# Kernel optimization log

Measured on AMD Instinct MI355X. Metric: run time of the kernel, lower is better.

The kernel has to match this reference:

```python
import jax, jax.numpy as jnp
import numpy as np

N, L, H1, H2 = 20000, 64, 128, 128  # nodes, max_len==input_dim, hidden_dim1, hidden_dim2


def setup_inputs() -> dict:
    key = jax.random.key(0)
    ks = jax.random.split(key, 12)
    sample_matrix = jax.random.normal(ks[0], (N, L, L), dtype=jnp.float32)
    sample_mask = jax.random.randint(ks[1], (N, L, L), 0, 2).astype(jnp.int32)
    sample_mask = sample_mask.at[:, :, 0].set(1)  # keep at least one valid logit per row
    # gather_idx[n, 0] = 0 (self prob); gather_idx[n, j] = position of node in neighbor j's list + 1
    gather_idx = jax.random.randint(ks[2], (N, L), 0, L).astype(jnp.int32)
    gather_idx = gather_idx.at[:, 0].set(0)
    # row_valid[n, j] = 1 iff j <= degree(n); rows past the degree stay 0 in middle_matrix
    row_valid = jax.random.randint(ks[3], (N, L), 0, 2).astype(jnp.int32)
    row_valid = row_valid.at[:, 0].set(1)
    s1 = np.float32(1.0 / np.sqrt(L))
    s2 = np.float32(1.0 / np.sqrt(H1))
    W1 = jax.random.normal(ks[4], (L, H1), dtype=jnp.float32) * s1
    b1 = jnp.zeros((H1,), jnp.float32)
    W2 = jax.random.normal(ks[5], (H1, L), dtype=jnp.float32) * s2
    b2 = jnp.zeros((L,), jnp.float32)
    W3 = jax.random.normal(ks[6], (L, H2), dtype=jnp.float32) * s1
    b3 = jnp.zeros((H2,), jnp.float32)
    W4 = jax.random.normal(ks[7], (H2, 1), dtype=jnp.float32) * s2
    b4 = jnp.zeros((1,), jnp.float32)
    return {
        "sample_matrix": sample_matrix, "sample_mask": sample_mask,
        "gather_idx": gather_idx, "row_valid": row_valid,
        "W1": W1, "b1": b1, "W2": W2, "b2": b2,
        "W3": W3, "b3": b3, "W4": W4, "b4": b4,
    }


def reference(sample_matrix, sample_mask, gather_idx, row_valid,
              W1, b1, W2, b2, W3, b3, W4, b4):
    # Per-(node,row) MLP: fc1 -> relu -> fc2, masked softmax over max_len (dropout is eval-mode identity)
    h = jax.nn.relu(jnp.einsum('nrk,kh->nrh', sample_matrix, W1) + b1)   # [N, L, H1]
    logits = jnp.einsum('nrh,hk->nrk', h, W2) + b2                        # [N, L, L]
    logits = jnp.where(sample_mask == 0, -jnp.inf, logits)
    probs = jax.nn.softmax(logits, axis=-1)                               # [N, L, L]
    # middle_matrix: row 0 takes prob[0], row j takes prob at the neighbor's back-pointer position
    mid = jnp.take_along_axis(probs, gather_idx[:, :, None], axis=2)[:, :, 0]  # [N, L]
    mid = jnp.where(row_valid == 1, mid, jnp.float32(0.0))                # unfilled rows stay 0
    mid = jnp.where(jnp.isnan(mid), jnp.float32(0.0), mid)                # all-masked softmax -> NaN -> 0
    y = jax.nn.relu(mid @ W3 + b3)                                        # [N, H2]
    out = jax.nn.sigmoid(y @ W4 + b4)                                     # [N, 1]
    return out.reshape(-1)
```

## Files before the change

kernel.cpp:

```cpp
#include <hip/hip_runtime.h>
#include <hip/hip_bf16.h>

typedef __attribute__((ext_vector_type(8))) __bf16 bf16x8;
typedef __attribute__((ext_vector_type(4))) float f32x4;

#define NN 20000
#define GRID1 1024
#define NSLOT 1024

__global__ void pack_w(const float* __restrict__ W1, const float* __restrict__ W2,
                       __bf16* __restrict__ w1p, __bf16* __restrict__ w2p) {
    int i = blockIdx.x * 256 + threadIdx.x;
    if (i < 64 * 128) {
        int c = i >> 6, k = i & 63;
        w1p[i] = (__bf16)W1[k * 128 + c];
        int c2 = i >> 7, k2 = i & 127;
        w2p[i] = (__bf16)W2[k2 * 64 + c2];
    }
}

struct NodeBuf { float4 sx[4]; int4 mv[4]; int gi; int rv; };

__global__ __launch_bounds__(256, 4) void vpsl_stage1p(
    const float* __restrict__ S, const int* __restrict__ mask,
    const int* __restrict__ gidx, const int* __restrict__ rvalid,
    const __bf16* __restrict__ w1p, const __bf16* __restrict__ w2p,
    const float* __restrict__ b1, const float* __restrict__ b2,
    float* __restrict__ midg)
{
    __shared__ __align__(16) __bf16 w1_lds[128 * 64];
    __shared__ __align__(16) __bf16 w2_lds[64 * 128];
    __shared__ __align__(16) __bf16 h_lds[4][16][136];

    const int tid  = threadIdx.x;
    const int w    = tid >> 6;
    const int lane = tid & 63;
    const int g    = lane >> 4;
    const int lc   = lane & 15;
    const int swz  = (lc & 7) << 4;

    for (int c = tid; c < 1024; c += 256) {
        int b = c * 16;
        int r1 = b >> 7, o1 = b & 127;
        *reinterpret_cast<float4*>(reinterpret_cast<char*>(w1_lds) + r1 * 128 + (o1 ^ ((r1 & 7) << 4)))
            = reinterpret_cast<const float4*>(w1p)[c];
        int r2 = b >> 8, o2 = b & 255;
        *reinterpret_cast<float4*>(reinterpret_cast<char*>(w2_lds) + r2 * 256 + (o2 ^ ((r2 & 7) << 4)))
            = reinterpret_cast<const float4*>(w2p)[c];
    }

    float b1v[8];
#pragma unroll
    for (int t = 0; t < 8; ++t) b1v[t] = b1[t * 16 + lc];
    float4 b2v4[4];
#pragma unroll
    for (int tm = 0; tm < 4; ++tm) b2v4[tm] = *reinterpret_cast<const float4*>(b2 + 16 * tm + 4 * g);

    __syncthreads();

    const int r = 16 * w + lc;
    const char* wc1 = reinterpret_cast<const char*>(w1_lds);
    const char* wc2 = reinterpret_cast<const char*>(w2_lds);

    auto LOADRV = [&](int2& rg, int node) {
        rg.x = rvalid[node * 64 + r];
        rg.y = gidx[node * 64 + r];
    };

    auto LOADNODE = [&](NodeBuf& nb, int node, int2 rg) {
        nb.rv = rg.x;
        nb.gi = rg.y;
        if (rg.x != 0) {
            const float* srow = S + ((size_t)node * 64 + r) * 64 + g * 8;
            nb.sx[0] = *reinterpret_cast<const float4*>(srow);
            nb.sx[1] = *reinterpret_cast<const float4*>(srow + 4);
            nb.sx[2] = *reinterpret_cast<const float4*>(srow + 32);
            nb.sx[3] = *reinterpret_cast<const float4*>(srow + 36);
            const int* mrow = mask + ((size_t)node * 64 + r) * 64 + 4 * g;
#pragma unroll
            for (int tm = 0; tm < 4; ++tm)
                nb.mv[tm] = *reinterpret_cast<const int4*>(mrow + 16 * tm);
        } else {
            float4 z4 = (float4){0.f, 0.f, 0.f, 0.f};
            int4   zi = (int4){0, 0, 0, 0};
#pragma unroll
            for (int q = 0; q < 4; ++q) { nb.sx[q] = z4; nb.mv[q] = zi; }
        }
    };

    auto COMPUTE = [&](const NodeBuf& nb, int node) {
        bf16x8 af[2];
#pragma unroll
        for (int ks = 0; ks < 2; ++ks) {
            bf16x8 a;
            a[0] = (__bf16)nb.sx[2 * ks].x; a[1] = (__bf16)nb.sx[2 * ks].y;
            a[2] = (__bf16)nb.sx[2 * ks].z; a[3] = (__bf16)nb.sx[2 * ks].w;
            a[4] = (__bf16)nb.sx[2 * ks + 1].x; a[5] = (__bf16)nb.sx[2 * ks + 1].y;
            a[6] = (__bf16)nb.sx[2 * ks + 1].z; a[7] = (__bf16)nb.sx[2 * ks + 1].w;
            af[ks] = a;
        }

#pragma unroll
        for (int t = 0; t < 8; ++t) {
            f32x4 acc = (f32x4){0.f, 0.f, 0.f, 0.f};
#pragma unroll
            for (int ks = 0; ks < 2; ++ks) {
                bf16x8 bw = *reinterpret_cast<const bf16x8*>(
                    wc1 + (t * 16 + lc) * 128 + ((ks * 64 + g * 16) ^ swz));
                acc = __builtin_amdgcn_mfma_f32_16x16x32_bf16(af[ks], bw, acc, 0, 0, 0);
            }
#pragma unroll
            for (int j = 0; j < 4; ++j) {
                float v = acc[j] + b1v[t];
                v = v > 0.f ? v : 0.f;
                h_lds[w][4 * g + j][16 * t + lc] = (__bf16)v;
            }
        }

        f32x4 lacc[4];
#pragma unroll
        for (int tm = 0; tm < 4; ++tm) lacc[tm] = (f32x4){0.f, 0.f, 0.f, 0.f};
#pragma unroll
        for (int ks = 0; ks < 4; ++ks) {
            bf16x8 ah = *reinterpret_cast<const bf16x8*>(&h_lds[w][lc][ks * 32 + g * 8]);
#pragma unroll
            for (int tm = 0; tm < 4; ++tm) {
                bf16x8 bw = *reinterpret_cast<const bf16x8*>(
                    wc2 + (tm * 16 + lc) * 256 + ((ks * 64 + g * 16) ^ swz));
                lacc[tm] = __builtin_amdgcn_mfma_f32_16x16x32_bf16(bw, ah, lacc[tm], 0, 0, 0);
            }
        }

        float l[4][4];
        float mt[4];
#pragma unroll
        for (int tm = 0; tm < 4; ++tm) {
            const int4  m4 = nb.mv[tm];
            const float4 bb = b2v4[tm];
            l[tm][0] = m4.x ? (lacc[tm][0] + bb.x) : -3.0e38f;
            l[tm][1] = m4.y ? (lacc[tm][1] + bb.y) : -3.0e38f;
            l[tm][2] = m4.z ? (lacc[tm][2] + bb.z) : -3.0e38f;
            l[tm][3] = m4.w ? (lacc[tm][3] + bb.w) : -3.0e38f;
            mt[tm] = fmaxf(fmaxf(l[tm][0], l[tm][1]), fmaxf(l[tm][2], l[tm][3]));
        }
        float mx = fmaxf(fmaxf(mt[0], mt[1]), fmaxf(mt[2], mt[3]));
        mx = fmaxf(mx, __shfl_xor(mx, 16));
        mx = fmaxf(mx, __shfl_xor(mx, 32));

        float st[4];
#pragma unroll
        for (int tm = 0; tm < 4; ++tm) {
#pragma unroll
            for (int j = 0; j < 4; ++j) l[tm][j] = __expf(l[tm][j] - mx);
            st[tm] = (l[tm][0] + l[tm][1]) + (l[tm][2] + l[tm][3]);
        }
        float s = (st[0] + st[1]) + (st[2] + st[3]);
        s += __shfl_xor(s, 16);
        s += __shfl_xor(s, 32);

        const int gi = nb.gi;
        float sel = 0.f;
#pragma unroll
        for (int tm = 0; tm < 4; ++tm)
#pragma unroll
            for (int j = 0; j < 4; ++j)
                sel += (gi == (16 * tm + 4 * g + j)) ? l[tm][j] : 0.f;
        sel += __shfl_xor(sel, 16);
        sel += __shfl_xor(sel, 32);

        if (g == 0) {
            float mval = (nb.rv != 0 && s > 0.f) ? (sel / s) : 0.f;
            midg[(size_t)node * 64 + r] = mval;
        }
    };

    int node = blockIdx.x;
    NodeBuf A, B;
    int2 rgA, rgB, rgT;
    rgT.x = 0; rgT.y = 0;
    LOADRV(rgA, node);
    if (node + NSLOT < NN) LOADRV(rgB, node + NSLOT); else { rgB.x = 0; rgB.y = 0; }
    LOADNODE(A, node, rgA);
    for (;;) {
        int n1 = node + NSLOT;
        int n2 = node + 2 * NSLOT;
        if (n2 < NN) LOADRV(rgT, n2);
        if (n1 < NN) LOADNODE(B, n1, rgB);
        COMPUTE(A, node);
        if (n1 >= NN) break;
        node = n1;
        n1 = node + NSLOT;
        n2 = node + 2 * NSLOT;
        if (n2 < NN) LOADRV(rgB, n2);
        if (n1 < NN) LOADNODE(A, n1, rgT);
        COMPUTE(B, node);
        if (n1 >= NN) break;
        node = n1;
    }
}

__global__ __launch_bounds__(256) void vpsl_stage2(
    const float* __restrict__ midg, const float* __restrict__ W3,
    const float* __restrict__ b3, const float* __restrict__ W4,
    const float* __restrict__ b4, float* __restrict__ out)
{
    __shared__ float mid_lds[2][64];
    __shared__ float red[2][128];
    const int tid = threadIdx.x;
    const int b = blockIdx.x;
    if (tid < 128) mid_lds[tid >> 6][tid & 63] = midg[(size_t)b * 128 + tid];
    __syncthreads();
    const int half = tid >> 7;
    const int t = tid & 127;
    float acc = 0.f;
#pragma unroll 8
    for (int k = 0; k < 64; ++k) acc += mid_lds[half][k] * W3[k * 128 + t];
    acc += b3[t];
    acc = acc > 0.f ? acc : 0.f;
    red[half][t] = acc * W4[t];
    __syncthreads();
    if ((tid & 127) < 64) {
        const int h2 = tid >> 7;
        const int tt = tid & 63;
        float v = red[h2][tt] + red[h2][tt + 64];
#pragma unroll
        for (int off = 1; off < 64; off <<= 1) v += __shfl_xor(v, off);
        if (tt == 0) out[b * 2 + h2] = 1.f / (1.f + __expf(-(v + b4[0])));
    }
}

__global__ __launch_bounds__(256) void vpsl_fused(
    const float* __restrict__ S, const int* __restrict__ mask,
    const int* __restrict__ gidx, const int* __restrict__ rvalid,
    const __bf16* __restrict__ w1p, const __bf16* __restrict__ w2p,
    const float* __restrict__ b1, const float* __restrict__ b2,
    const float* __restrict__ W3, const float* __restrict__ b3,
    const float* __restrict__ W4, const float* __restrict__ b4,
    float* __restrict__ out)
{
    __shared__ __align__(16) __bf16 h_lds[4][16][136];
    __shared__ float mid_s[64];
    __shared__ int   gi_s[64];
    __shared__ int   rv_s[64];
    __shared__ float red_s[128];

    const int n    = blockIdx.x;
    const int tid  = threadIdx.x;
    const int w    = tid >> 6;
    const int lane = tid & 63;
    const int g    = lane >> 4;
    const int lc   = lane & 15;

    if (tid < 64) {
        gi_s[tid] = gidx[(size_t)n * 64 + tid];
        rv_s[tid] = rvalid[(size_t)n * 64 + tid];
    }
    float b1v[8];
#pragma unroll
    for (int t = 0; t < 8; ++t) b1v[t] = b1[t * 16 + lc];
    float b2v[4];
#pragma unroll
    for (int t = 0; t < 4; ++t) b2v[t] = b2[t * 16 + lc];

    const float* srow = S + ((size_t)n * 64 + 16 * w + lc) * 64;
    bf16x8 af[2];
#pragma unroll
    for (int ks = 0; ks < 2; ++ks) {
        const float4* p = reinterpret_cast<const float4*>(srow + ks * 32 + g * 8);
        float4 x0 = p[0], x1 = p[1];
        bf16x8 a;
        a[0] = (__bf16)x0.x; a[1] = (__bf16)x0.y; a[2] = (__bf16)x0.z; a[3] = (__bf16)x0.w;
        a[4] = (__bf16)x1.x; a[5] = (__bf16)x1.y; a[6] = (__bf16)x1.z; a[7] = (__bf16)x1.w;
        af[ks] = a;
    }
    f32x4 hacc[8];
#pragma unroll
    for (int t = 0; t < 8; ++t) hacc[t] = (f32x4){0.f, 0.f, 0.f, 0.f};
#pragma unroll
    for (int ks = 0; ks < 2; ++ks)
#pragma unroll
        for (int t = 0; t < 8; ++t) {
            bf16x8 bf = *reinterpret_cast<const bf16x8*>(w1p + (t * 16 + lc) * 64 + ks * 32 + g * 8);
            hacc[t] = __builtin_amdgcn_mfma_f32_16x16x32_bf16(af[ks], bf, hacc[t], 0, 0, 0);
        }
#pragma unroll
    for (int t = 0; t < 8; ++t)
#pragma unroll
        for (int j = 0; j < 4; ++j) {
            float v = hacc[t][j] + b1v[t];
            v = v > 0.f ? v : 0.f;
            h_lds[w][4 * g + j][16 * t + lc] = (__bf16)v;
        }
    __syncthreads();

    f32x4 lacc[4];
#pragma unroll
    for (int t = 0; t < 4; ++t) lacc[t] = (f32x4){0.f, 0.f, 0.f, 0.f};
#pragma unroll
    for (int ks = 0; ks < 4; ++ks) {
        bf16x8 ah = *reinterpret_cast<const bf16x8*>(&h_lds[w][lc][ks * 32 + g * 8]);
#pragma unroll
        for (int t = 0; t < 4; ++t) {
            bf16x8 bf = *reinterpret_cast<const bf16x8*>(w2p + (t * 16 + lc) * 128 + ks * 32 + g * 8);
            lacc[t] = __builtin_amdgcn_mfma_f32_16x16x32_bf16(ah, bf, lacc[t], 0, 0, 0);
        }
    }
#pragma unroll
    for (int j = 0; j < 4; ++j) {
        const int row = 16 * w + 4 * g + j;
        const int* mrow = mask + ((size_t)n * 64 + row) * 64 + lc;
        int m[4];
#pragma unroll
        for (int t = 0; t < 4; ++t) m[t] = mrow[16 * t];
        float l[4];
#pragma unroll
        for (int t = 0; t < 4; ++t) l[t] = m[t] ? (lacc[t][j] + b2v[t]) : -3.0e38f;
        float mx = fmaxf(fmaxf(l[0], l[1]), fmaxf(l[2], l[3]));
#pragma unroll
        for (int off = 1; off < 16; off <<= 1) mx = fmaxf(mx, __shfl_xor(mx, off));
        float e[4];
#pragma unroll
        for (int t = 0; t < 4; ++t) e[t] = m[t] ? __expf(l[t] - mx) : 0.f;
        float s = (e[0] + e[1]) + (e[2] + e[3]);
#pragma unroll
        for (int off = 1; off < 16; off <<= 1) s += __shfl_xor(s, off);
        const int gi = gi_s[row];
        float sel = 0.f;
#pragma unroll
        for (int t = 0; t < 4; ++t) sel += (((gi >> 4) == t) && ((gi & 15) == lc)) ? e[t] : 0.f;
#pragma unroll
        for (int off = 1; off < 16; off <<= 1) sel += __shfl_xor(sel, off);
        if (lc == 0) {
            float mval = (rv_s[row] != 0 && s > 0.f) ? (sel / s) : 0.f;
            mid_s[row] = mval;
        }
    }
    __syncthreads();

    if (tid < 128) {
        float acc = 0.f;
#pragma unroll 8
        for (int k = 0; k < 64; ++k) acc += mid_s[k] * W3[k * 128 + tid];
        acc += b3[tid];
        acc = acc > 0.f ? acc : 0.f;
        red_s[tid] = acc * W4[tid];
    }
    __syncthreads();
    if (tid < 64) {
        float v = red_s[tid] + red_s[tid + 64];
#pragma unroll
        for (int off = 1; off < 64; off <<= 1) v += __shfl_xor(v, off);
        if (tid == 0) out[n] = 1.f / (1.f + __expf(-(v + b4[0])));
    }
}

extern "C" void kernel_launch(void* const* d_in, const int* in_sizes, int n_in,
                              void* d_out, int out_size, void* d_ws, size_t ws_size,
                              hipStream_t stream) {
    const float* S    = (const float*)d_in[0];
    const int*   mask = (const int*)d_in[1];
    const int*   gidx = (const int*)d_in[2];
    const int*   rv   = (const int*)d_in[3];
    const float* W1   = (const float*)d_in[4];
    const float* b1   = (const float*)d_in[5];
    const float* W2   = (const float*)d_in[6];
    const float* b2   = (const float*)d_in[7];
    const float* W3   = (const float*)d_in[8];
    const float* b3   = (const float*)d_in[9];
    const float* W4   = (const float*)d_in[10];
    const float* b4   = (const float*)d_in[11];
    float* out = (float*)d_out;

    __bf16* w1p = (__bf16*)d_ws;
    __bf16* w2p = w1p + 64 * 128;
    float*  midg = (float*)(w2p + 64 * 128);

    const size_t need = 2 * 64 * 128 * sizeof(__bf16) + (size_t)NN * 64 * sizeof(float);

    hipLaunchKernelGGL(pack_w, dim3(32), dim3(256), 0, stream, W1, W2, w1p, w2p);
    if (ws_size >= need) {
        hipLaunchKernelGGL(vpsl_stage1p, dim3(GRID1), dim3(256), 0, stream,
                           S, mask, gidx, rv, w1p, w2p, b1, b2, midg);
        hipLaunchKernelGGL(vpsl_stage2, dim3(NN / 2), dim3(256), 0, stream,
                           midg, W3, b3, W4, b4, out);
    } else {
        hipLaunchKernelGGL(vpsl_fused, dim3(NN), dim3(256), 0, stream,
                           S, mask, gidx, rv, w1p, w2p, b1, b2, W3, b3, W4, b4, out);
    }
}
```

Measured before the change: 143.9 us.

## Keep MLP weight fragments in registers instead of LDS, halve persistent grid

Loads the bf16 W1 and W2 MFMA operand fragments straight into per-thread registers (32 bf16x8 vectors) and drops the LDS weight copies, the swizzle and the block barrier. It also folds the b1/b2 bias adds into the MFMA accumulator initialisation. To fit the extra register pressure, launch bounds drop from 4 to 2 blocks per CU and the persistent grid is halved to 512 blocks. This removes LDS read traffic for the weights in the inner loop, at the cost of lower occupancy and less latency hiding for the streaming global loads.

After: 307.2 us. 114% more time.

```diff
diff --git a/kernel.cpp b/kernel.cpp
--- a/kernel.cpp
+++ b/kernel.cpp
@@ -5,8 +5,8 @@
 typedef __attribute__((ext_vector_type(4))) float f32x4;
 
 #define NN 20000
-#define GRID1 1024
-#define NSLOT 1024
+#define GRID1 512
+#define NSLOT 512
 
 __global__ void pack_w(const float* __restrict__ W1, const float* __restrict__ W2,
                        __bf16* __restrict__ w1p, __bf16* __restrict__ w2p) {
@@ -21,15 +21,13 @@
 
 struct NodeBuf { float4 sx[4]; int4 mv[4]; int gi; int rv; };
 
-__global__ __launch_bounds__(256, 4) void vpsl_stage1p(
+__global__ __launch_bounds__(256, 2) void vpsl_stage1p(
     const float* __restrict__ S, const int* __restrict__ mask,
     const int* __restrict__ gidx, const int* __restrict__ rvalid,
     const __bf16* __restrict__ w1p, const __bf16* __restrict__ w2p,
     const float* __restrict__ b1, const float* __restrict__ b2,
     float* __restrict__ midg)
 {
-    __shared__ __align__(16) __bf16 w1_lds[128 * 64];
-    __shared__ __align__(16) __bf16 w2_lds[64 * 128];
     __shared__ __align__(16) __bf16 h_lds[4][16][136];
 
     const int tid  = threadIdx.x;
@@ -37,17 +35,19 @@
     const int lane = tid & 63;
     const int g    = lane >> 4;
     const int lc   = lane & 15;
-    const int swz  = (lc & 7) << 4;
-
-    for (int c = tid; c < 1024; c += 256) {
-        int b = c * 16;
-        int r1 = b >> 7, o1 = b & 127;
-        *reinterpret_cast<float4*>(reinterpret_cast<char*>(w1_lds) + r1 * 128 + (o1 ^ ((r1 & 7) << 4)))
-            = reinterpret_cast<const float4*>(w1p)[c];
-        int r2 = b >> 8, o2 = b & 255;
-        *reinterpret_cast<float4*>(reinterpret_cast<char*>(w2_lds) + r2 * 256 + (o2 ^ ((r2 & 7) << 4)))
-            = reinterpret_cast<const float4*>(w2p)[c];
-    }
+
+    bf16x8 w1f[16];
+#pragma unroll
+    for (int t = 0; t < 8; ++t)
+#pragma unroll
+        for (int ks = 0; ks < 2; ++ks)
+            w1f[t * 2 + ks] = *reinterpret_cast<const bf16x8*>(w1p + (t * 16 + lc) * 64 + ks * 32 + g * 8);
+    bf16x8 w2f[16];
+#pragma unroll
+    for (int ks = 0; ks < 4; ++ks)
+#pragma unroll
+        for (int tm = 0; tm < 4; ++tm)
+            w2f[ks * 4 + tm] = *reinterpret_cast<const bf16x8*>(w2p + (tm * 16 + lc) * 128 + ks * 32 + g * 8);
 
     float b1v[8];
 #pragma unroll
@@ -56,11 +56,7 @@
 #pragma unroll
     for (int tm = 0; tm < 4; ++tm) b2v4[tm] = *reinterpret_cast<const float4*>(b2 + 16 * tm + 4 * g);
 
-    __syncthreads();
-
     const int r = 16 * w + lc;
-    const char* wc1 = reinterpret_cast<const char*>(w1_lds);
-    const char* wc2 = reinterpret_cast<const char*>(w2_lds);
 
     auto LOADRV = [&](int2& rg, int node) {
         rg.x = rvalid[node * 64 + r];
@@ -102,45 +98,37 @@
 
 #pragma unroll
         for (int t = 0; t < 8; ++t) {
-            f32x4 acc = (f32x4){0.f, 0.f, 0.f, 0.f};
-#pragma unroll
-            for (int ks = 0; ks < 2; ++ks) {
-                bf16x8 bw = *reinterpret_cast<const bf16x8*>(
-                    wc1 + (t * 16 + lc) * 128 + ((ks * 64 + g * 16) ^ swz));
-                acc = __builtin_amdgcn_mfma_f32_16x16x32_bf16(af[ks], bw, acc, 0, 0, 0);
-            }
+            f32x4 acc = (f32x4){b1v[t], b1v[t], b1v[t], b1v[t]};
+            acc = __builtin_amdgcn_mfma_f32_16x16x32_bf16(af[0], w1f[t * 2 + 0], acc, 0, 0, 0);
+            acc = __builtin_amdgcn_mfma_f32_16x16x32_bf16(af[1], w1f[t * 2 + 1], acc, 0, 0, 0);
 #pragma unroll
             for (int j = 0; j < 4; ++j) {
-                float v = acc[j] + b1v[t];
-                v = v > 0.f ? v : 0.f;
+                float v = acc[j] > 0.f ? acc[j] : 0.f;
                 h_lds[w][4 * g + j][16 * t + lc] = (__bf16)v;
             }
         }
 
         f32x4 lacc[4];
 #pragma unroll
-        for (int tm = 0; tm < 4; ++tm) lacc[tm] = (f32x4){0.f, 0.f, 0.f, 0.f};
+        for (int tm = 0; tm < 4; ++tm)
+            lacc[tm] = (f32x4){b2v4[tm].x, b2v4[tm].y, b2v4[tm].z, b2v4[tm].w};
 #pragma unroll
         for (int ks = 0; ks < 4; ++ks) {
             bf16x8 ah = *reinterpret_cast<const bf16x8*>(&h_lds[w][lc][ks * 32 + g * 8]);
 #pragma unroll
-            for (int tm = 0; tm < 4; ++tm) {
-                bf16x8 bw = *reinterpret_cast<const bf16x8*>(
-                    wc2 + (tm * 16 + lc) * 256 + ((ks * 64 + g * 16) ^ swz));
-                lacc[tm] = __builtin_amdgcn_mfma_f32_16x16x32_bf16(bw, ah, lacc[tm], 0, 0, 0);
-            }
+            for (int tm = 0; tm < 4; ++tm)
+                lacc[tm] = __builtin_amdgcn_mfma_f32_16x16x32_bf16(w2f[ks * 4 + tm], ah, lacc[tm], 0, 0, 0);
         }
 
         float l[4][4];
         float mt[4];
 #pragma unroll
         for (int tm = 0; tm < 4; ++tm) {
-            const int4  m4 = nb.mv[tm];
-            const float4 bb = b2v4[tm];
-            l[tm][0] = m4.x ? (lacc[tm][0] + bb.x) : -3.0e38f;
-            l[tm][1] = m4.y ? (lacc[tm][1] + bb.y) : -3.0e38f;
-            l[tm][2] = m4.z ? (lacc[tm][2] + bb.z) : -3.0e38f;
-            l[tm][3] = m4.w ? (lacc[tm][3] + bb.w) : -3.0e38f;
+            const int4 m4 = nb.mv[tm];
+            l[tm][0] = m4.x ? lacc[tm][0] : -3.0e38f;
+            l[tm][1] = m4.y ? lacc[tm][1] : -3.0e38f;
+            l[tm][2] = m4.z ? lacc[tm][2] : -3.0e38f;
+            l[tm][3] = m4.w ? lacc[tm][3] : -3.0e38f;
             mt[tm] = fmaxf(fmaxf(l[tm][0], l[tm][1]), fmaxf(l[tm][2], l[tm][3]));
         }
         float mx = fmaxf(fmaxf(mt[0], mt[1]), fmaxf(mt[2], mt[3]));
```
